# Performance work log

Hardware: AMD Instinct MI355X
Metric: run time of the kernel (lower is better)

The kernel has to match this reference:

```python
import jax, jax.numpy as jnp
import numpy as np

TOP_K = 2
ROUTING_SCALE = 1.0
SCORE_FUNC = 'softmax'  # matches init_kwargs


def setup_inputs() -> dict:
    key = jax.random.key(0)
    k1, k2 = jax.random.split(key)
    x = jax.random.normal(k1, (16384, 2048), dtype=jnp.float32)
    # router weight: nn.Linear(hidden, experts).weight has shape [experts, hidden], init std=0.02
    W = jax.random.normal(k2, (64, 2048), dtype=jnp.float32) * 0.02
    return {"x": x, "W": W}


def reference(x, W):
    # scores = x @ W.T : [tokens, num_experts]
    scores = jnp.einsum('th,eh->te', x, W)
    # original_scores is detached in the torch code
    original_scores = jax.lax.stop_gradient(scores)
    if SCORE_FUNC == 'softmax':
        probs = jax.nn.softmax(scores, axis=-1)
    else:
        probs = jax.nn.sigmoid(scores)
    # top-k over experts (torch uses sorted=False; selected set/values identical)
    _, top_k_indices = jax.lax.top_k(probs, TOP_K)
    routing_weights = jnp.take_along_axis(original_scores, top_k_indices, axis=-1)
    if SCORE_FUNC == 'sigmoid':
        routing_weights = routing_weights / (routing_weights.sum(axis=-1, keepdims=True) + 1e-06)
    routing_weights = routing_weights * ROUTING_SCALE
    return routing_weights, top_k_indices
```

## Files before the change

kernel.cpp:

```cpp
#include <hip/hip_runtime.h>
#include <stdint.h>

#define KDIM 2048
#define NEXP 64
#define MT   64
#define KC   32
#define NTHR 256
#define NTOK 16384

typedef _Float16 half8 __attribute__((ext_vector_type(8)));
typedef __fp16  fp16x2 __attribute__((ext_vector_type(2)));
typedef float f32x4 __attribute__((ext_vector_type(4)));

__device__ __forceinline__ int swz(int row, int byte_in_row) {
    return ((row << 6) + byte_in_row) ^ ((row & 14) << 3);
}

__device__ __forceinline__ uint32_t pkrtz(float a, float b) {
    fp16x2 h = __builtin_amdgcn_cvt_pkrtz(a, b);
    return __builtin_bit_cast(uint32_t, h);
}

__device__ __forceinline__ void split4(float4 v, uint2* hv, uint2* lv) {
    float y[4] = {v.x, v.y, v.z, v.w};
    uint32_t hw[2], lw[2];
    #pragma unroll
    for (int i = 0; i < 2; ++i) {
        float y0 = y[2 * i], y1 = y[2 * i + 1];
        float h0 = __builtin_bit_cast(float, __builtin_bit_cast(uint32_t, y0) & 0xFFFFE000u);
        float h1 = __builtin_bit_cast(float, __builtin_bit_cast(uint32_t, y1) & 0xFFFFE000u);
        hw[i] = pkrtz(h0, h1);
        lw[i] = pkrtz(y0 - h0, y1 - h1);
    }
    hv->x = hw[0]; hv->y = hw[1];
    lv->x = lw[0]; lv->y = lw[1];
}

#define VMCNT4() do { asm volatile("s_waitcnt vmcnt(4)" ::: "memory"); \
                      __builtin_amdgcn_sched_barrier(0); } while (0)
#define VMCNT0() do { asm volatile("s_waitcnt vmcnt(0)" ::: "memory"); \
                      __builtin_amdgcn_sched_barrier(0); } while (0)
#define LGKM_BAR() do { asm volatile("s_waitcnt lgkmcnt(0)" ::: "memory"); \
                        __builtin_amdgcn_sched_barrier(0);                 \
                        __builtin_amdgcn_s_barrier();                      \
                        __builtin_amdgcn_sched_barrier(0); } while (0)

__global__ __launch_bounds__(NTHR) void router_kernel(const float* __restrict__ x,
                                                      const float* __restrict__ W,
                                                      float* __restrict__ partials) {
    __shared__ char AsB[2][2][4096];
    __shared__ char BsB[2][2][4096];

    const int tid  = threadIdx.x;
    const int lane = tid & 63;
    const int wave = tid >> 6;
    const int wm   = wave >> 1;
    const int wn   = wave & 1;
    const int kh   = blockIdx.x & 1;
    const int tb   = (blockIdx.x >> 1) * MT;
    const int kb0  = kh * (KDIM / 2);

    const int xrow0 = tid >> 3;
    const int xseg  = tid & 7;
    const float* xsrc0 = x + (size_t)(tb + xrow0) * KDIM + kb0 + xseg * 4;
    const float* xsrc1 = x + (size_t)(tb + xrow0 + 32) * KDIM + kb0 + xseg * 4;
    const int xoff0 = swz(xrow0, xseg * 8);
    const int xoff1 = swz(xrow0 + 32, xseg * 8);
    const int wrr = tid >> 2;
    const int wss = tid & 3;
    const float* wsrc = W + (size_t)wrr * KDIM + kb0 + wss * 8;
    const int woff = swz(wrr, wss * 16);

    const int kb = lane >> 4;
    const int ra0 = wm * 32 + (lane & 15);
    const int rb0 = wn * 32 + (lane & 15);
    const int aoff0 = swz(ra0,      kb * 16);
    const int aoff1 = swz(ra0 + 16, kb * 16);
    const int boff0 = swz(rb0,      kb * 16);
    const int boff1 = swz(rb0 + 16, kb * 16);

    f32x4 acc[2][2];
    #pragma unroll
    for (int i = 0; i < 2; ++i)
        #pragma unroll
        for (int j = 0; j < 2; ++j)
            acc[i][j] = (f32x4){0.f, 0.f, 0.f, 0.f};

    float4 Ax0, Ax1, Aw0, Aw1;
    float4 Bx0, Bx1, Bw0, Bw1;

#define LOADM(X0, X1, W0, W1, c)                                           \
    do {                                                                   \
        X0 = *reinterpret_cast<const float4*>(xsrc0 + (c) * KC);           \
        X1 = *reinterpret_cast<const float4*>(xsrc1 + (c) * KC);           \
        W0 = *reinterpret_cast<const float4*>(wsrc + (c) * KC);            \
        W1 = *reinterpret_cast<const float4*>(wsrc + (c) * KC + 4);        \
    } while (0)

    auto STORE = [&](int b, float4 v0, float4 v1, float4 w0, float4 w1) {
        uint2 hv, lv;
        split4(v0, &hv, &lv);
        *reinterpret_cast<uint2*>(&AsB[b][0][0] + xoff0) = hv;
        *reinterpret_cast<uint2*>(&AsB[b][1][0] + xoff0) = lv;
        split4(v1, &hv, &lv);
        *reinterpret_cast<uint2*>(&AsB[b][0][0] + xoff1) = hv;
        *reinterpret_cast<uint2*>(&AsB[b][1][0] + xoff1) = lv;
        uint2 h0, l0, h1, l1;
        split4(w0, &h0, &l0);
        split4(w1, &h1, &l1);
        uint4 wh = {h0.x, h0.y, h1.x, h1.y};
        uint4 wl = {l0.x, l0.y, l1.x, l1.y};
        *reinterpret_cast<uint4*>(&BsB[b][0][0] + woff) = wh;
        *reinterpret_cast<uint4*>(&BsB[b][1][0] + woff) = wl;
    };

    auto COMPUTE = [&](int b) {
        half8 ah[2], al[2], bh[2], bl[2];
        ah[0] = *reinterpret_cast<const half8*>(&AsB[b][0][0] + aoff0);
        ah[1] = *reinterpret_cast<const half8*>(&AsB[b][0][0] + aoff1);
        al[0] = *reinterpret_cast<const half8*>(&AsB[b][1][0] + aoff0);
        al[1] = *reinterpret_cast<const half8*>(&AsB[b][1][0] + aoff1);
        bh[0] = *reinterpret_cast<const half8*>(&BsB[b][0][0] + boff0);
        bh[1] = *reinterpret_cast<const half8*>(&BsB[b][0][0] + boff1);
        bl[0] = *reinterpret_cast<const half8*>(&BsB[b][1][0] + boff0);
        bl[1] = *reinterpret_cast<const half8*>(&BsB[b][1][0] + boff1);
        #pragma unroll
        for (int m = 0; m < 2; ++m)
            #pragma unroll
            for (int n = 0; n < 2; ++n) {
                acc[m][n] = __builtin_amdgcn_mfma_f32_16x16x32_f16(ah[m], bh[n], acc[m][n], 0, 0, 0);
                acc[m][n] = __builtin_amdgcn_mfma_f32_16x16x32_f16(al[m], bh[n], acc[m][n], 0, 0, 0);
                acc[m][n] = __builtin_amdgcn_mfma_f32_16x16x32_f16(ah[m], bl[n], acc[m][n], 0, 0, 0);
            }
    };

    LOADM(Ax0, Ax1, Aw0, Aw1, 0);
    LOADM(Bx0, Bx1, Bw0, Bw1, 1);
    VMCNT4();
    STORE(0, Ax0, Ax1, Aw0, Aw1);
    LGKM_BAR();

    for (int q = 0; q < 15; ++q) {
        COMPUTE(0);
        LOADM(Ax0, Ax1, Aw0, Aw1, 2 * q + 2);
        VMCNT4();
        STORE(1, Bx0, Bx1, Bw0, Bw1);
        LGKM_BAR();
        COMPUTE(1);
        LOADM(Bx0, Bx1, Bw0, Bw1, 2 * q + 3);
        VMCNT4();
        STORE(0, Ax0, Ax1, Aw0, Aw1);
        LGKM_BAR();
    }
    COMPUTE(0);
    VMCNT0();
    STORE(1, Bx0, Bx1, Bw0, Bw1);
    LGKM_BAR();
    COMPUTE(1);

    float* pbase = partials + (size_t)kh * NTOK * NEXP;
    #pragma unroll
    for (int m = 0; m < 2; ++m)
        #pragma unroll
        for (int n = 0; n < 2; ++n)
            #pragma unroll
            for (int r = 0; r < 4; ++r) {
                int tok = wm * 32 + m * 16 + (lane >> 4) * 4 + r;
                int e   = wn * 32 + n * 16 + (lane & 15);
                pbase[(size_t)(tb + tok) * NEXP + e] = acc[m][n][r];
            }
#undef LOADM
}

__global__ __launch_bounds__(256) void reduce_kernel(const float* __restrict__ partials,
                                                     float* __restrict__ out_w,
                                                     float* __restrict__ out_i) {
    const int t = blockIdx.x * 256 + threadIdx.x;
    const float4* p0 = reinterpret_cast<const float4*>(partials + (size_t)t * NEXP);
    const float4* p1 = reinterpret_cast<const float4*>(partials + (size_t)NTOK * NEXP + (size_t)t * NEXP);
    float s[NEXP];
    #pragma unroll
    for (int j = 0; j < NEXP / 4; ++j) {
        float4 a = p0[j];
        float4 b = p1[j];
        s[4 * j + 0] = a.x + b.x;
        s[4 * j + 1] = a.y + b.y;
        s[4 * j + 2] = a.z + b.z;
        s[4 * j + 3] = a.w + b.w;
    }
    float m1 = -1e30f, m2 = -1e30f;
    int i1 = 0, i2 = 0;
    #pragma unroll
    for (int e = 0; e < NEXP; ++e) {
        float v = s[e];
        if (v > m1) { m2 = m1; i2 = i1; m1 = v; i1 = e; }
        else if (v > m2) { m2 = v; i2 = e; }
    }
    out_w[t * 2 + 0] = m1;
    out_w[t * 2 + 1] = m2;
    out_i[t * 2 + 0] = (float)i1;
    out_i[t * 2 + 1] = (float)i2;
}

extern "C" void kernel_launch(void* const* d_in, const int* in_sizes, int n_in,
                              void* d_out, int out_size, void* d_ws, size_t ws_size,
                              hipStream_t stream) {
    const float* x = (const float*)d_in[0];
    const float* W = (const float*)d_in[1];
    float* out = (float*)d_out;

    const int n_tokens = in_sizes[0] / KDIM;
    float* partials = (float*)d_ws;

    hipLaunchKernelGGL(router_kernel, dim3((n_tokens / MT) * 2), dim3(NTHR), 0, stream,
                       x, W, partials);
    hipLaunchKernelGGL(reduce_kernel, dim3(n_tokens / 256), dim3(256), 0, stream,
                       partials, out, out + 2 * (size_t)n_tokens);
}
```

Baseline: 35.06 us.

## Fuse split-K reduction and top-2 selection into router GEMM via in-block K halves

Each block now has 512 threads split into two groups that each handle one K half for the same 64-token tile. The partial sums are combined in shared memory and top-2 selection is done inside the same kernel. This removes the global partials round trip and the second kernel launch. In exchange the grid is halved, the block is larger with twice the shared memory, and only 64 threads run the top-k tail.

```diff
diff --git a/kernel.cpp b/kernel.cpp
--- a/kernel.cpp
+++ b/kernel.cpp
@@ -5,7 +5,7 @@
 #define NEXP 64
 #define MT   64
 #define KC   32
-#define NTHR 256
+#define NTHR 512
 #define NTOK 16384
 
 typedef _Float16 half8 __attribute__((ext_vector_type(8)));
@@ -47,27 +47,29 @@
 
 __global__ __launch_bounds__(NTHR) void router_kernel(const float* __restrict__ x,
                                                       const float* __restrict__ W,
-                                                      float* __restrict__ partials) {
-    __shared__ char AsB[2][2][4096];
-    __shared__ char BsB[2][2][4096];
+                                                      float* __restrict__ out_w,
+                                                      float* __restrict__ out_i) {
+    __shared__ char AsB[2][2][2][4096];
+    __shared__ char BsB[2][2][2][4096];
 
     const int tid  = threadIdx.x;
     const int lane = tid & 63;
     const int wave = tid >> 6;
-    const int wm   = wave >> 1;
+    const int g    = wave >> 2;
+    const int wm   = (wave >> 1) & 1;
     const int wn   = wave & 1;
-    const int kh   = blockIdx.x & 1;
-    const int tb   = (blockIdx.x >> 1) * MT;
-    const int kb0  = kh * (KDIM / 2);
-
-    const int xrow0 = tid >> 3;
-    const int xseg  = tid & 7;
+    const int tidg = tid & 255;
+    const int tb   = blockIdx.x * MT;
+    const int kb0  = g * (KDIM / 2);
+
+    const int xrow0 = tidg >> 3;
+    const int xseg  = tidg & 7;
     const float* xsrc0 = x + (size_t)(tb + xrow0) * KDIM + kb0 + xseg * 4;
     const float* xsrc1 = x + (size_t)(tb + xrow0 + 32) * KDIM + kb0 + xseg * 4;
     const int xoff0 = swz(xrow0, xseg * 8);
     const int xoff1 = swz(xrow0 + 32, xseg * 8);
-    const int wrr = tid >> 2;
-    const int wss = tid & 3;
+    const int wrr = tidg >> 2;
+    const int wss = tidg & 3;
     const float* wsrc = W + (size_t)wrr * KDIM + kb0 + wss * 8;
     const int woff = swz(wrr, wss * 16);
 
@@ -100,30 +102,30 @@
     auto STORE = [&](int b, float4 v0, float4 v1, float4 w0, float4 w1) {
         uint2 hv, lv;
         split4(v0, &hv, &lv);
-        *reinterpret_cast<uint2*>(&AsB[b][0][0] + xoff0) = hv;
-        *reinterpret_cast<uint2*>(&AsB[b][1][0] + xoff0) = lv;
+        *reinterpret_cast<uint2*>(&AsB[g][b][0][0] + xoff0) = hv;
+        *reinterpret_cast<uint2*>(&AsB[g][b][1][0] + xoff0) = lv;
         split4(v1, &hv, &lv);
-        *reinterpret_cast<uint2*>(&AsB[b][0][0] + xoff1) = hv;
-        *reinterpret_cast<uint2*>(&AsB[b][1][0] + xoff1) = lv;
+        *reinterpret_cast<uint2*>(&AsB[g][b][0][0] + xoff1) = hv;
+        *reinterpret_cast<uint2*>(&AsB[g][b][1][0] + xoff1) = lv;
         uint2 h0, l0, h1, l1;
         split4(w0, &h0, &l0);
         split4(w1, &h1, &l1);
         uint4 wh = {h0.x, h0.y, h1.x, h1.y};
         uint4 wl = {l0.x, l0.y, l1.x, l1.y};
-        *reinterpret_cast<uint4*>(&BsB[b][0][0] + woff) = wh;
-        *reinterpret_cast<uint4*>(&BsB[b][1][0] + woff) = wl;
+        *reinterpret_cast<uint4*>(&BsB[g][b][0][0] + woff) = wh;
+        *reinterpret_cast<uint4*>(&BsB[g][b][1][0] + woff) = wl;
     };
 
     auto COMPUTE = [&](int b) {
         half8 ah[2], al[2], bh[2], bl[2];
-        ah[0] = *reinterpret_cast<const half8*>(&AsB[b][0][0] + aoff0);
-        ah[1] = *reinterpret_cast<const half8*>(&AsB[b][0][0] + aoff1);
-        al[0] = *reinterpret_cast<const half8*>(&AsB[b][1][0] + aoff0);
-        al[1] = *reinterpret_cast<const half8*>(&AsB[b][1][0] + aoff1);
-        bh[0] = *reinterpret_cast<const half8*>(&BsB[b][0][0] + boff0);
-        bh[1] = *reinterpret_cast<const half8*>(&BsB[b][0][0] + boff1);
-        bl[0] = *reinterpret_cast<const half8*>(&BsB[b][1][0] + boff0);
-        bl[1] = *reinterpret_cast<const half8*>(&BsB[b][1][0] + boff1);
+        ah[0] = *reinterpret_cast<const half8*>(&AsB[g][b][0][0] + aoff0);
+        ah[1] = *reinterpret_cast<const half8*>(&AsB[g][b][0][0] + aoff1);
+        al[0] = *reinterpret_cast<const half8*>(&AsB[g][b][1][0] + aoff0);
+        al[1] = *reinterpret_cast<const half8*>(&AsB[g][b][1][0] + aoff1);
+        bh[0] = *reinterpret_cast<const half8*>(&BsB[g][b][0][0] + boff0);
+        bh[1] = *reinterpret_cast<const half8*>(&BsB[g][b][0][0] + boff1);
+        bl[0] = *reinterpret_cast<const half8*>(&BsB[g][b][1][0] + boff0);
+        bl[1] = *reinterpret_cast<const half8*>(&BsB[g][b][1][0] + boff1);
         #pragma unroll
         for (int m = 0; m < 2; ++m)
             #pragma unroll
@@ -158,48 +160,52 @@
     LGKM_BAR();
     COMPUTE(1);
 
-    float* pbase = partials + (size_t)kh * NTOK * NEXP;
-    #pragma unroll
-    for (int m = 0; m < 2; ++m)
-        #pragma unroll
-        for (int n = 0; n < 2; ++n)
+    __syncthreads();
+    float (*ss)[NEXP + 3] = reinterpret_cast<float (*)[NEXP + 3]>(&AsB[0][0][0][0]);
+    if (g == 0) {
+        #pragma unroll
+        for (int m = 0; m < 2; ++m)
             #pragma unroll
-            for (int r = 0; r < 4; ++r) {
-                int tok = wm * 32 + m * 16 + (lane >> 4) * 4 + r;
-                int e   = wn * 32 + n * 16 + (lane & 15);
-                pbase[(size_t)(tb + tok) * NEXP + e] = acc[m][n][r];
-            }
+            for (int n = 0; n < 2; ++n)
+                #pragma unroll
+                for (int r = 0; r < 4; ++r) {
+                    int tok = wm * 32 + m * 16 + (lane >> 4) * 4 + r;
+                    int e   = wn * 32 + n * 16 + (lane & 15);
+                    ss[tok][e] = acc[m][n][r];
+                }
+    }
+    __syncthreads();
+    if (g == 1) {
+        #pragma unroll
+        for (int m = 0; m < 2; ++m)
+            #pragma unroll
+            for (int n = 0; n < 2; ++n)
+                #pragma unroll
+                for (int r = 0; r < 4; ++r) {
+                    int tok = wm * 32 + m * 16 + (lane >> 4) * 4 + r;
+                    int e   = wn * 32 + n * 16 + (lane & 15);
+                    ss[tok][e] += acc[m][n][r];
+                }
+    }
+    __syncthreads();
+
+    if (tid < MT) {
+        const int t = tid;
+        float m1 = -1e30f, m2 = -1e30f;
+        int i1 = 0, i2 = 0;
+        #pragma unroll
+        for (int e = 0; e < NEXP; ++e) {
+            float v = ss[t][e];
+            if (v > m1) { m2 = m1; i2 = i1; m1 = v; i1 = e; }
+            else if (v > m2) { m2 = v; i2 = e; }
+        }
+        const int gt = tb + t;
+        out_w[gt * 2 + 0] = m1;
+        out_w[gt * 2 + 1] = m2;
+        out_i[gt * 2 + 0] = (float)i1;
+        out_i[gt * 2 + 1] = (float)i2;
+    }
 #undef LOADM
-}
-
-__global__ __launch_bounds__(256) void reduce_kernel(const float* __restrict__ partials,
-                                                     float* __restrict__ out_w,
-                                                     float* __restrict__ out_i) {
-    const int t = blockIdx.x * 256 + threadIdx.x;
-    const float4* p0 = reinterpret_cast<const float4*>(partials + (size_t)t * NEXP);
-    const float4* p1 = reinterpret_cast<const float4*>(partials + (size_t)NTOK * NEXP + (size_t)t * NEXP);
-    float s[NEXP];
-    #pragma unroll
-    for (int j = 0; j < NEXP / 4; ++j) {
-        float4 a = p0[j];
-        float4 b = p1[j];
-        s[4 * j + 0] = a.x + b.x;
-        s[4 * j + 1] = a.y + b.y;
-        s[4 * j + 2] = a.z + b.z;
-        s[4 * j + 3] = a.w + b.w;
-    }
-    float m1 = -1e30f, m2 = -1e30f;
-    int i1 = 0, i2 = 0;
-    #pragma unroll
-    for (int e = 0; e < NEXP; ++e) {
-        float v = s[e];
-        if (v > m1) { m2 = m1; i2 = i1; m1 = v; i1 = e; }
-        else if (v > m2) { m2 = v; i2 = e; }
-    }
-    out_w[t * 2 + 0] = m1;
-    out_w[t * 2 + 1] = m2;
-    out_i[t * 2 + 0] = (float)i1;
-    out_i[t * 2 + 1] = (float)i2;
 }
 
 extern "C" void kernel_launch(void* const* d_in, const int* in_sizes, int n_in,
@@ -210,10 +216,7 @@
     float* out = (float*)d_out;
 
     const int n_tokens = in_sizes[0] / KDIM;
-    float* partials = (float*)d_ws;
-
-    hipLaunchKernelGGL(router_kernel, dim3((n_tokens / MT) * 2), dim3(NTHR), 0, stream,
-                       x, W, partials);
-    hipLaunchKernelGGL(reduce_kernel, dim3(n_tokens / 256), dim3(256), 0, stream,
-                       partials, out, out + 2 * (size_t)n_tokens);
-}
+
+    hipLaunchKernelGGL(router_kernel, dim3(n_tokens / MT), dim3(NTHR), 0, stream,
+                       x, W, out, out + 2 * (size_t)n_tokens);
+}
```

New measurement: 31.27 us, median of 2. 1.12x faster.
